# Performance work log

Measured on AMD Instinct MI355X. Metric: run time of the kernel, lower is better.

Reference implementation:

```python
import jax, jax.numpy as jnp
import numpy as np

L, WIDTH, H, B, S = 3, 4, 512, 32, 512
NHW = 2
CIN = (WIDTH + 1) * H


def _windows(padded, off0):
    # padded: [B, S+2W, H] -> [B, S, (W+1)*H], window k covers padded[:, off0+k : off0+k+S]
    return jnp.concatenate([padded[:, off0 + k: off0 + k + S] for k in range(WIDTH + 1)], axis=-1)


def _highway(x, Ws, bs):
    # Ws: [NHW, H, 2H], bs: [NHW, 2H]. AllenNLP Highway: gate*x + (1-gate)*relu(nonlin)
    for j in range(NHW):
        proj = x @ Ws[j] + bs[j]
        nonlin, gate = jnp.split(proj, 2, axis=-1)
        g = jax.nn.sigmoid(gate)
        x = g * x + (1.0 - g) * jax.nn.relu(nonlin)
    return x


def setup_inputs() -> dict:
    key = jax.random.key(0)
    ks = jax.random.split(key, 13)
    inputs = jax.random.normal(ks[0], (B, S, H), dtype=jnp.float32)
    mask = jnp.ones((B, S), dtype=jnp.int32)
    fwd_pads = jax.random.normal(ks[1], (L, WIDTH, H), dtype=jnp.float32)
    bwd_pads = jax.random.normal(ks[2], (L, WIDTH, H), dtype=jnp.float32)
    fwd_W = jax.random.normal(ks[3], (L, CIN, H), dtype=jnp.float32) * 0.02
    bwd_W = jax.random.normal(ks[4], (L, CIN, H), dtype=jnp.float32) * 0.02
    fwd_b = jnp.zeros((L, H), dtype=jnp.float32)
    bwd_b = jnp.zeros((L, H), dtype=jnp.float32)
    fwd_hw_W = jax.random.normal(ks[5], (L, NHW, H, 2 * H), dtype=jnp.float32) * 0.04
    bwd_hw_W = jax.random.normal(ks[6], (L, NHW, H, 2 * H), dtype=jnp.float32) * 0.04
    fwd_hw_b = jnp.zeros((L, NHW, 2 * H), dtype=jnp.float32)
    bwd_hw_b = jnp.zeros((L, NHW, 2 * H), dtype=jnp.float32)
    return {"inputs": inputs, "mask": mask, "fwd_pads": fwd_pads, "bwd_pads": bwd_pads,
            "fwd_W": fwd_W, "fwd_b": fwd_b, "bwd_W": bwd_W, "bwd_b": bwd_b,
            "fwd_hw_W": fwd_hw_W, "fwd_hw_b": fwd_hw_b, "bwd_hw_W": bwd_hw_W, "bwd_hw_b": bwd_hw_b}


def reference(inputs, mask, fwd_pads, bwd_pads, fwd_W, fwd_b, bwd_W, bwd_b,
              fwd_hw_W, fwd_hw_b, bwd_hw_W, bwd_hw_b):
    f_seq = inputs
    b_seq = inputs
    outs = []
    for i in range(L):
        pf = jnp.broadcast_to(fwd_pads[i], (B, WIDTH, H))
        pb = jnp.broadcast_to(bwd_pads[i], (B, WIDTH, H))
        pad_f = jnp.concatenate([pf, f_seq, pb], axis=1)  # [B, S+2W, H]
        pad_b = jnp.concatenate([pf, b_seq, pb], axis=1)
        # forward windows start at offset 0 (positions t-W..t); backward at offset W (t..t+W)
        f_in = _windows(pad_f, 0)       # [B, S, (W+1)*H]
        b_in = _windows(pad_b, WIDTH)
        f = jax.nn.relu(f_in @ fwd_W[i] + fwd_b[i])
        f = _highway(f, fwd_hw_W[i], fwd_hw_b[i])
        b = jax.nn.relu(b_in @ bwd_W[i] + bwd_b[i])
        b = _highway(b, bwd_hw_W[i], bwd_hw_b[i])
        f_seq, b_seq = f, b
        outs.append(jnp.concatenate([f, b], axis=-1))
    return jnp.stack(outs, axis=0)  # [L, B, S, 2H]
```

## Files before the change

kernel.cpp:

```cpp
#include <hip/hip_runtime.h>
#include <hip/hip_fp16.h>
#include <cstdint>
#include <cstddef>

constexpr int HD   = 512;
constexpr int SQ   = 512;
constexpr int NB   = 32;
constexpr int LAY  = 3;
constexpr int WID  = 4;
constexpr int KIN  = (WID + 1) * HD;
constexpr int PROW = SQ + 2 * WID;
constexpr int MR   = NB * SQ;

typedef _Float16 f16x8 __attribute__((ext_vector_type(8)));
typedef float    f32x4 __attribute__((ext_vector_type(4)));

__device__ __forceinline__ void gld16(void* lds, const void* g) {
  __builtin_amdgcn_global_load_lds(
      (__attribute__((address_space(1))) void*)(g),
      (__attribute__((address_space(3))) void*)(lds),
      16, 0, 0);
}

__global__ void transpose_w(const float* __restrict__ in, _Float16* __restrict__ out,
                            int R, int C) {
  __shared__ float tile[32][33];
  const size_t base = (size_t)blockIdx.z * R * C;
  const int r0 = blockIdx.y * 32, c0 = blockIdx.x * 32;
  const int tx = threadIdx.x, ty = threadIdx.y;
#pragma unroll
  for (int j = 0; j < 32; j += 8)
    tile[ty + j][tx] = in[base + (size_t)(r0 + ty + j) * C + (c0 + tx)];
  __syncthreads();
#pragma unroll
  for (int j = 0; j < 32; j += 8)
    out[base + (size_t)(c0 + ty + j) * R + (r0 + tx)] = (_Float16)tile[tx][ty + j];
}

__global__ void init_interior(const float4* __restrict__ in,
                              _Float16* __restrict__ padF, _Float16* __restrict__ padB) {
  const size_t idx = (size_t)blockIdx.x * 256 + threadIdx.x;
  float4 v = in[idx];
  const size_t e = idx * 4;
  const int h = (int)(e & (HD - 1));
  const size_t bt = e >> 9;
  const int t = (int)(bt & (SQ - 1));
  const int b = (int)(bt >> 9);
  const size_t o = ((size_t)(b * PROW + WID + t)) * HD + h;
  union { _Float16 hh[4]; uint2 u; } pk;
  pk.hh[0] = (_Float16)v.x; pk.hh[1] = (_Float16)v.y;
  pk.hh[2] = (_Float16)v.z; pk.hh[3] = (_Float16)v.w;
  *(uint2*)&padF[o] = pk.u;
  *(uint2*)&padB[o] = pk.u;
}

__global__ void fill_pads(const float* __restrict__ fpad, const float* __restrict__ bpad,
                          _Float16* __restrict__ padF, _Float16* __restrict__ padB) {
  const int idx = blockIdx.x * 256 + threadIdx.x;
  const int h  = idx & (HD - 1);
  const int w  = (idx >> 9) & 3;
  const int b  = (idx >> 11) & 31;
  const int fb = idx >> 16;
  const float v = fb ? bpad[w * HD + h] : fpad[w * HD + h];
  const int row = fb ? (SQ + WID + w) : w;
  const size_t o = ((size_t)(b * PROW + row)) * HD + h;
  const _Float16 hv = (_Float16)v;
  padF[o] = hv;
  padB[o] = hv;
}

__global__ __launch_bounds__(256)
void conv_gemm(const _Float16* __restrict__ padFp, const _Float16* __restrict__ padBp,
               const _Float16* __restrict__ WtF, const _Float16* __restrict__ WtB,
               const float* __restrict__ biasF, const float* __restrict__ biasB,
               _Float16* __restrict__ tF, _Float16* __restrict__ tB) {
  const int id   = blockIdx.x;
  const int xcd  = id & 7;
  const int dir  = xcd >> 2;
  const int xl   = xcd & 3;
  const int slot = id >> 3;
  const int nt   = slot & 3;
  const int mg   = slot >> 2;
  const int mt   = xl + 4 * mg;

  const _Float16* pad = dir ? padBp : padFp;
  const _Float16* Wt  = dir ? WtB : WtF;
  const float* bias   = dir ? biasB : biasF;
  _Float16* outT      = dir ? tB : tF;
  const int off = dir ? WID : 0;

  const int m0 = mt * 128;
  const int n0 = nt * 128;
  const int b  = m0 >> 9;
  const int t0 = m0 & (SQ - 1);

  __shared__ alignas(16) _Float16 Asm[128 * 64];
  __shared__ alignas(16) _Float16 Bsm[128 * 64];

  const int tid  = threadIdx.x;
  const int lane = tid & 63, wv = tid >> 6;
  const int wr = (wv >> 1) * 64, wc = (wv & 1) * 64;
  const int lr = lane & 15, q = lane >> 4;
  const int srow = tid >> 3;
  const int clog = (tid & 7) ^ (srow & 7);
  const int goff = clog * 8;

  f32x4 acc[4][4] = {};

  const size_t arow0 = (size_t)(b * PROW + t0 + off);

#pragma unroll 2
  for (int k0 = 0; k0 < KIN; k0 += 64) {
    const int kseg = k0 >> 9;
    const int h0 = k0 & (HD - 1);
    const _Float16* Ab = pad + (arow0 + kseg) * (size_t)HD + h0;
    const _Float16* Bb = Wt + (size_t)n0 * KIN + k0;
    __syncthreads();
#pragma unroll
    for (int j = 0; j < 4; ++j) {
      gld16(&Asm[j * 2048 + tid * 8], Ab + (size_t)(j * 32 + srow) * HD + goff);
      gld16(&Bsm[j * 2048 + tid * 8], Bb + (size_t)(j * 32 + srow) * KIN + goff);
    }
    __syncthreads();

#pragma unroll
    for (int h = 0; h < 2; ++h) {
      f16x8 af[4], bf[4];
#pragma unroll
      for (int r = 0; r < 4; ++r) {
        const int row = wr + r * 16 + lr;
        const int ch = ((h << 2) | q) ^ (lr & 7);
        af[r] = *(const f16x8*)&Asm[row * 64 + ch * 8];
      }
#pragma unroll
      for (int c = 0; c < 4; ++c) {
        const int row = wc + c * 16 + lr;
        const int ch = ((h << 2) | q) ^ (lr & 7);
        bf[c] = *(const f16x8*)&Bsm[row * 64 + ch * 8];
      }
#pragma unroll
      for (int r = 0; r < 4; ++r)
#pragma unroll
        for (int c = 0; c < 4; ++c)
          acc[r][c] = __builtin_amdgcn_mfma_f32_16x16x32_f16(af[r], bf[c], acc[r][c], 0, 0, 0);
    }
  }

#pragma unroll
  for (int c = 0; c < 4; ++c) {
    const int ng = n0 + wc + c * 16 + lr;
    const float bv = bias[ng];
#pragma unroll
    for (int r = 0; r < 4; ++r) {
      const int mg2 = m0 + wr + r * 16 + q * 4;
#pragma unroll
      for (int g = 0; g < 4; ++g) {
        float v = acc[r][c][g] + bv;
        v = v > 0.f ? v : 0.f;
        outT[(size_t)(mg2 + g) * HD + ng] = (_Float16)v;
      }
    }
  }
}

__global__ __launch_bounds__(256)
void hw_gemm(const _Float16* __restrict__ xF, const _Float16* __restrict__ xB,
             const _Float16* __restrict__ WtFp, const _Float16* __restrict__ WtBp,
             const float* __restrict__ bFp, const float* __restrict__ bBp,
             _Float16* __restrict__ oFp, _Float16* __restrict__ oBp,
             float* __restrict__ out32, int mode) {
  const int id   = blockIdx.x;
  const int xcd  = id & 7;
  const int dir  = xcd >> 2;
  const int xl   = xcd & 3;
  const int slot = id >> 3;
  const int nt   = slot & 7;
  const int mg   = slot >> 3;
  const int mt   = xl + 4 * mg;

  const _Float16* x  = dir ? xB : xF;
  const _Float16* Wt = dir ? WtBp : WtFp;
  const float* bias  = dir ? bBp : bFp;
  _Float16* oh       = dir ? oBp : oFp;

  const int m0 = mt * 128;
  const int n0 = nt * 64;

  __shared__ alignas(16) _Float16 Asm[128 * 64];
  __shared__ alignas(16) _Float16 Bn[64 * 64];
  __shared__ alignas(16) _Float16 Bg[64 * 64];

  const int tid  = threadIdx.x;
  const int lane = tid & 63, wv = tid >> 6;
  const int wr = (wv >> 1) * 64, wc = (wv & 1) * 32;
  const int lr = lane & 15, q = lane >> 4;
  const int srow = tid >> 3;
  const int clog = (tid & 7) ^ (srow & 7);
  const int goff = clog * 8;

  f32x4 an[4][2] = {};
  f32x4 ag[4][2] = {};
  _Float16 xv[4][2][4] = {};

  for (int k0 = 0; k0 < HD; k0 += 64) {
    const _Float16* Ab  = x + (size_t)m0 * HD + k0;
    const _Float16* Bnb = Wt + (size_t)n0 * HD + k0;
    const _Float16* Bgb = Wt + (size_t)(HD + n0) * HD + k0;
    __syncthreads();
#pragma unroll
    for (int j = 0; j < 4; ++j)
      gld16(&Asm[j * 2048 + tid * 8], Ab + (size_t)(j * 32 + srow) * HD + goff);
#pragma unroll
    for (int j = 0; j < 2; ++j) {
      gld16(&Bn[j * 2048 + tid * 8], Bnb + (size_t)(j * 32 + srow) * HD + goff);
      gld16(&Bg[j * 2048 + tid * 8], Bgb + (size_t)(j * 32 + srow) * HD + goff);
    }
    __syncthreads();

    if (k0 == n0) {
#pragma unroll
      for (int r = 0; r < 4; ++r)
#pragma unroll
        for (int c = 0; c < 2; ++c)
#pragma unroll
          for (int g = 0; g < 4; ++g) {
            const int row = wr + r * 16 + q * 4 + g;
            const int col = wc + c * 16 + lr;
            xv[r][c][g] = Asm[row * 64 + ((((col >> 3) ^ (row & 7)) << 3) | (col & 7))];
          }
    }

#pragma unroll
    for (int h = 0; h < 2; ++h) {
      f16x8 af[4], bn[2], bg[2];
#pragma unroll
      for (int r = 0; r < 4; ++r) {
        const int row = wr + r * 16 + lr;
        const int ch = ((h << 2) | q) ^ (lr & 7);
        af[r] = *(const f16x8*)&Asm[row * 64 + ch * 8];
      }
#pragma unroll
      for (int c = 0; c < 2; ++c) {
        const int row = wc + c * 16 + lr;
        const int ch = ((h << 2) | q) ^ (lr & 7);
        bn[c] = *(const f16x8*)&Bn[row * 64 + ch * 8];
        bg[c] = *(const f16x8*)&Bg[row * 64 + ch * 8];
      }
#pragma unroll
      for (int r = 0; r < 4; ++r)
#pragma unroll
        for (int c = 0; c < 2; ++c) {
          an[r][c] = __builtin_amdgcn_mfma_f32_16x16x32_f16(af[r], bn[c], an[r][c], 0, 0, 0);
          ag[r][c] = __builtin_amdgcn_mfma_f32_16x16x32_f16(af[r], bg[c], ag[r][c], 0, 0, 0);
        }
    }
  }

#pragma unroll
  for (int c = 0; c < 2; ++c) {
    const int ng = n0 + wc + c * 16 + lr;
    const float bnv = bias[ng];
    const float bgv = bias[HD + ng];
#pragma unroll
    for (int r = 0; r < 4; ++r) {
      const int mg2 = m0 + wr + r * 16 + q * 4;
#pragma unroll
      for (int g = 0; g < 4; ++g) {
        const int row = mg2 + g;
        float nl = an[r][c][g] + bnv;
        nl = nl > 0.f ? nl : 0.f;
        const float gz = ag[r][c][g] + bgv;
        const float gate = 1.f / (1.f + __expf(-gz));
        const float xvf = (float)xv[r][c][g];
        const float o = gate * xvf + (1.f - gate) * nl;
        if (mode == 0) {
          oh[(size_t)row * HD + ng] = (_Float16)o;
        } else {
          const int bb = row >> 9, tt = row & (SQ - 1);
          oh[((size_t)(bb * PROW + WID + tt)) * HD + ng] = (_Float16)o;
          out32[(size_t)row * (2 * HD) + dir * HD + ng] = o;
        }
      }
    }
  }
}

extern "C" void kernel_launch(void* const* d_in, const int* in_sizes, int n_in,
                              void* d_out, int out_size, void* d_ws, size_t ws_size,
                              hipStream_t stream) {
  const float* inputs   = (const float*)d_in[0];
  const float* fwd_pads = (const float*)d_in[2];
  const float* bwd_pads = (const float*)d_in[3];
  const float* fwd_W    = (const float*)d_in[4];
  const float* fwd_b    = (const float*)d_in[5];
  const float* bwd_W    = (const float*)d_in[6];
  const float* bwd_b    = (const float*)d_in[7];
  const float* fwd_hw_W = (const float*)d_in[8];
  const float* fwd_hw_b = (const float*)d_in[9];
  const float* bwd_hw_W = (const float*)d_in[10];
  const float* bwd_hw_b = (const float*)d_in[11];
  float* out = (float*)d_out;

  char* p = (char*)d_ws;
  auto take = [&](size_t n) { char* r = p; p += (n + 255) & ~(size_t)255; return r; };

  _Float16* padF = (_Float16*)take((size_t)NB * PROW * HD * 2);
  _Float16* padB = (_Float16*)take((size_t)NB * PROW * HD * 2);
  _Float16* tF   = (_Float16*)take((size_t)MR * HD * 2);
  _Float16* tB   = (_Float16*)take((size_t)MR * HD * 2);
  _Float16* uF   = (_Float16*)take((size_t)MR * HD * 2);
  _Float16* uB   = (_Float16*)take((size_t)MR * HD * 2);
  _Float16* WtcF = (_Float16*)take((size_t)LAY * HD * KIN * 2);
  _Float16* WtcB = (_Float16*)take((size_t)LAY * HD * KIN * 2);
  _Float16* WthF = (_Float16*)take((size_t)LAY * 2 * (2 * HD) * HD * 2);
  _Float16* WthB = (_Float16*)take((size_t)LAY * 2 * (2 * HD) * HD * 2);

  transpose_w<<<dim3(HD / 32, KIN / 32, LAY), dim3(32, 8), 0, stream>>>(fwd_W, WtcF, KIN, HD);
  transpose_w<<<dim3(HD / 32, KIN / 32, LAY), dim3(32, 8), 0, stream>>>(bwd_W, WtcB, KIN, HD);
  transpose_w<<<dim3((2 * HD) / 32, HD / 32, LAY * 2), dim3(32, 8), 0, stream>>>(fwd_hw_W, WthF, HD, 2 * HD);
  transpose_w<<<dim3((2 * HD) / 32, HD / 32, LAY * 2), dim3(32, 8), 0, stream>>>(bwd_hw_W, WthB, HD, 2 * HD);

  init_interior<<<(NB * SQ * HD / 4) / 256, 256, 0, stream>>>((const float4*)inputs, padF, padB);

  for (int i = 0; i < LAY; ++i) {
    fill_pads<<<512, 256, 0, stream>>>(fwd_pads + (size_t)i * WID * HD,
                                       bwd_pads + (size_t)i * WID * HD, padF, padB);
    conv_gemm<<<dim3(1024), 256, 0, stream>>>(
        padF, padB,
        WtcF + (size_t)i * HD * KIN, WtcB + (size_t)i * HD * KIN,
        fwd_b + (size_t)i * HD, bwd_b + (size_t)i * HD, tF, tB);
    hw_gemm<<<dim3(2048), 256, 0, stream>>>(
        tF, tB,
        WthF + (size_t)(i * 2 + 0) * (2 * HD) * HD, WthB + (size_t)(i * 2 + 0) * (2 * HD) * HD,
        fwd_hw_b + (size_t)(i * 2 + 0) * (2 * HD), bwd_hw_b + (size_t)(i * 2 + 0) * (2 * HD),
        uF, uB, nullptr, 0);
    hw_gemm<<<dim3(2048), 256, 0, stream>>>(
        uF, uB,
        WthF + (size_t)(i * 2 + 1) * (2 * HD) * HD, WthB + (size_t)(i * 2 + 1) * (2 * HD) * HD,
        fwd_hw_b + (size_t)(i * 2 + 1) * (2 * HD), bwd_hw_b + (size_t)(i * 2 + 1) * (2 * HD),
        padF, padB, out + (size_t)i * MR * (2 * HD), 1);
  }
}
```

Measured before the change: 1.071 ms.

## Enlarge highway GEMM tiles, stage epilogues through LDS, and batch setup kernels

The highway GEMM now uses 256x64 output tiles, each wave covering 64 rows by all 64 columns, and launches half as many blocks. Both GEMM epilogues write results to swizzled LDS first, then issue 16-byte coalesced global stores. The highway residual is now read from global memory in the epilogue instead of being captured from LDS in the K loop. Setup is batched: the forward and backward weight transposes share one launch, and the pad rows for all layers are filled once into per-layer pad buffers, which removes the per-layer fill kernel. The last layer skips writing the unused padded copy. The trade-offs are more LDS per block and the gate pre-activation being rounded to fp16 before the sigmoid.

```diff
diff --git a/kernel.cpp b/kernel.cpp
--- a/kernel.cpp
+++ b/kernel.cpp
@@ -11,6 +11,7 @@
 constexpr int KIN  = (WID + 1) * HD;
 constexpr int PROW = SQ + 2 * WID;
 constexpr int MR   = NB * SQ;
+constexpr int PSTR = NB * PROW * HD;
 
 typedef _Float16 f16x8 __attribute__((ext_vector_type(8)));
 typedef float    f32x4 __attribute__((ext_vector_type(4)));
@@ -22,10 +23,15 @@
       16, 0, 0);
 }
 
-__global__ void transpose_w(const float* __restrict__ in, _Float16* __restrict__ out,
-                            int R, int C) {
+__global__ void transpose_w2(const float* __restrict__ inF, const float* __restrict__ inB,
+                             _Float16* __restrict__ outF, _Float16* __restrict__ outB,
+                             int R, int C, int nsl) {
   __shared__ float tile[32][33];
-  const size_t base = (size_t)blockIdx.z * R * C;
+  const int z = blockIdx.z;
+  const float* in = (z < nsl) ? inF : inB;
+  _Float16* out   = (z < nsl) ? outF : outB;
+  const int sl    = (z < nsl) ? z : z - nsl;
+  const size_t base = (size_t)sl * R * C;
   const int r0 = blockIdx.y * 32, c0 = blockIdx.x * 32;
   const int tx = threadIdx.x, ty = threadIdx.y;
 #pragma unroll
@@ -54,16 +60,17 @@
   *(uint2*)&padB[o] = pk.u;
 }
 
-__global__ void fill_pads(const float* __restrict__ fpad, const float* __restrict__ bpad,
-                          _Float16* __restrict__ padF, _Float16* __restrict__ padB) {
+__global__ void fill_all_pads(const float* __restrict__ fpads, const float* __restrict__ bpads,
+                              _Float16* __restrict__ padF, _Float16* __restrict__ padB) {
   const int idx = blockIdx.x * 256 + threadIdx.x;
   const int h  = idx & (HD - 1);
   const int w  = (idx >> 9) & 3;
   const int b  = (idx >> 11) & 31;
-  const int fb = idx >> 16;
-  const float v = fb ? bpad[w * HD + h] : fpad[w * HD + h];
+  const int fb = (idx >> 16) & 1;
+  const int l  = idx >> 17;
+  const float v = fb ? bpads[l * WID * HD + w * HD + h] : fpads[l * WID * HD + w * HD + h];
   const int row = fb ? (SQ + WID + w) : w;
-  const size_t o = ((size_t)(b * PROW + row)) * HD + h;
+  const size_t o = (size_t)l * PSTR + ((size_t)(b * PROW + row)) * HD + h;
   const _Float16 hv = (_Float16)v;
   padF[o] = hv;
   padB[o] = hv;
@@ -94,8 +101,9 @@
   const int b  = m0 >> 9;
   const int t0 = m0 & (SQ - 1);
 
-  __shared__ alignas(16) _Float16 Asm[128 * 64];
-  __shared__ alignas(16) _Float16 Bsm[128 * 64];
+  __shared__ alignas(16) _Float16 SM[128 * 128];
+  _Float16* Asm = SM;
+  _Float16* Bsm = SM + 8192;
 
   const int tid  = threadIdx.x;
   const int lane = tid & 63, wv = tid >> 6;
@@ -126,18 +134,13 @@
 #pragma unroll
     for (int h = 0; h < 2; ++h) {
       f16x8 af[4], bf[4];
-#pragma unroll
-      for (int r = 0; r < 4; ++r) {
-        const int row = wr + r * 16 + lr;
-        const int ch = ((h << 2) | q) ^ (lr & 7);
-        af[r] = *(const f16x8*)&Asm[row * 64 + ch * 8];
-      }
-#pragma unroll
-      for (int c = 0; c < 4; ++c) {
-        const int row = wc + c * 16 + lr;
-        const int ch = ((h << 2) | q) ^ (lr & 7);
-        bf[c] = *(const f16x8*)&Bsm[row * 64 + ch * 8];
-      }
+      const int ch = ((h << 2) | q) ^ (lr & 7);
+#pragma unroll
+      for (int r = 0; r < 4; ++r)
+        af[r] = *(const f16x8*)&Asm[(wr + r * 16 + lr) * 64 + ch * 8];
+#pragma unroll
+      for (int c = 0; c < 4; ++c)
+        bf[c] = *(const f16x8*)&Bsm[(wc + c * 16 + lr) * 64 + ch * 8];
 #pragma unroll
       for (int r = 0; r < 4; ++r)
 #pragma unroll
@@ -146,20 +149,31 @@
     }
   }
 
+  __syncthreads();
 #pragma unroll
   for (int c = 0; c < 4; ++c) {
-    const int ng = n0 + wc + c * 16 + lr;
-    const float bv = bias[ng];
-#pragma unroll
-    for (int r = 0; r < 4; ++r) {
-      const int mg2 = m0 + wr + r * 16 + q * 4;
+    const int col = wc + c * 16 + lr;
+    const float bv = bias[n0 + col];
+#pragma unroll
+    for (int r = 0; r < 4; ++r)
 #pragma unroll
       for (int g = 0; g < 4; ++g) {
+        const int row = wr + r * 16 + q * 4 + g;
+        const int pc = (col >> 3) ^ (row & 7);
         float v = acc[r][c][g] + bv;
         v = v > 0.f ? v : 0.f;
-        outT[(size_t)(mg2 + g) * HD + ng] = (_Float16)v;
+        SM[row * 128 + pc * 8 + (col & 7)] = (_Float16)v;
       }
-    }
+  }
+  __syncthreads();
+#pragma unroll
+  for (int j = 0; j < 8; ++j) {
+    const int cid = j * 256 + tid;
+    const int row = cid >> 4;
+    const int gc = cid & 15;
+    const int pc = gc ^ (row & 7);
+    f16x8 v8 = *(const f16x8*)&SM[row * 128 + pc * 8];
+    *(f16x8*)&outT[(size_t)(m0 + row) * HD + n0 + gc * 8] = v8;
   }
 }
 
@@ -183,32 +197,32 @@
   const float* bias  = dir ? bBp : bFp;
   _Float16* oh       = dir ? oBp : oFp;
 
-  const int m0 = mt * 128;
+  const int m0 = mt * 256;
   const int n0 = nt * 64;
 
-  __shared__ alignas(16) _Float16 Asm[128 * 64];
-  __shared__ alignas(16) _Float16 Bn[64 * 64];
-  __shared__ alignas(16) _Float16 Bg[64 * 64];
+  __shared__ alignas(16) _Float16 SM[32768];
+  _Float16* Asm = SM;
+  _Float16* Bn  = SM + 16384;
+  _Float16* Bg  = SM + 20480;
 
   const int tid  = threadIdx.x;
   const int lane = tid & 63, wv = tid >> 6;
-  const int wr = (wv >> 1) * 64, wc = (wv & 1) * 32;
   const int lr = lane & 15, q = lane >> 4;
   const int srow = tid >> 3;
   const int clog = (tid & 7) ^ (srow & 7);
   const int goff = clog * 8;
 
-  f32x4 an[4][2] = {};
-  f32x4 ag[4][2] = {};
-  _Float16 xv[4][2][4] = {};
-
+  f32x4 an[4][4] = {};
+  f32x4 ag[4][4] = {};
+
+#pragma unroll 2
   for (int k0 = 0; k0 < HD; k0 += 64) {
     const _Float16* Ab  = x + (size_t)m0 * HD + k0;
     const _Float16* Bnb = Wt + (size_t)n0 * HD + k0;
     const _Float16* Bgb = Wt + (size_t)(HD + n0) * HD + k0;
     __syncthreads();
 #pragma unroll
-    for (int j = 0; j < 4; ++j)
+    for (int j = 0; j < 8; ++j)
       gld16(&Asm[j * 2048 + tid * 8], Ab + (size_t)(j * 32 + srow) * HD + goff);
 #pragma unroll
     for (int j = 0; j < 2; ++j) {
@@ -217,70 +231,77 @@
     }
     __syncthreads();
 
-    if (k0 == n0) {
+#pragma unroll
+    for (int h = 0; h < 2; ++h) {
+      const int ch = ((h << 2) | q) ^ (lr & 7);
+      f16x8 af[4], bn[4], bg[4];
 #pragma unroll
       for (int r = 0; r < 4; ++r)
-#pragma unroll
-        for (int c = 0; c < 2; ++c)
-#pragma unroll
-          for (int g = 0; g < 4; ++g) {
-            const int row = wr + r * 16 + q * 4 + g;
-            const int col = wc + c * 16 + lr;
-            xv[r][c][g] = Asm[row * 64 + ((((col >> 3) ^ (row & 7)) << 3) | (col & 7))];
-          }
-    }
-
-#pragma unroll
-    for (int h = 0; h < 2; ++h) {
-      f16x8 af[4], bn[2], bg[2];
-#pragma unroll
-      for (int r = 0; r < 4; ++r) {
-        const int row = wr + r * 16 + lr;
-        const int ch = ((h << 2) | q) ^ (lr & 7);
-        af[r] = *(const f16x8*)&Asm[row * 64 + ch * 8];
+        af[r] = *(const f16x8*)&Asm[(wv * 64 + r * 16 + lr) * 64 + ch * 8];
+#pragma unroll
+      for (int c = 0; c < 4; ++c) {
+        bn[c] = *(const f16x8*)&Bn[(c * 16 + lr) * 64 + ch * 8];
+        bg[c] = *(const f16x8*)&Bg[(c * 16 + lr) * 64 + ch * 8];
       }
 #pragma unroll
-      for (int c = 0; c < 2; ++c) {
-        const int row = wc + c * 16 + lr;
-        const int ch = ((h << 2) | q) ^ (lr & 7);
-        bn[c] = *(const f16x8*)&Bn[row * 64 + ch * 8];
-        bg[c] = *(const f16x8*)&Bg[row * 64 + ch * 8];
-      }
-#pragma unroll
       for (int r = 0; r < 4; ++r)
 #pragma unroll
-        for (int c = 0; c < 2; ++c) {
+        for (int c = 0; c < 4; ++c) {
           an[r][c] = __builtin_amdgcn_mfma_f32_16x16x32_f16(af[r], bn[c], an[r][c], 0, 0, 0);
           ag[r][c] = __builtin_amdgcn_mfma_f32_16x16x32_f16(af[r], bg[c], ag[r][c], 0, 0, 0);
         }
     }
   }
 
-#pragma unroll
-  for (int c = 0; c < 2; ++c) {
-    const int ng = n0 + wc + c * 16 + lr;
-    const float bnv = bias[ng];
-    const float bgv = bias[HD + ng];
-#pragma unroll
-    for (int r = 0; r < 4; ++r) {
-      const int mg2 = m0 + wr + r * 16 + q * 4;
+  __syncthreads();
+#pragma unroll
+  for (int c = 0; c < 4; ++c) {
+    const int col = c * 16 + lr;
+    const float bnv = bias[n0 + col];
+    const float bgv = bias[HD + n0 + col];
+#pragma unroll
+    for (int r = 0; r < 4; ++r)
 #pragma unroll
       for (int g = 0; g < 4; ++g) {
-        const int row = mg2 + g;
+        const int row = wv * 64 + r * 16 + q * 4 + g;
+        const int pc = (col >> 3) ^ (row & 7);
+        const int a = row * 64 + pc * 8 + (col & 7);
         float nl = an[r][c][g] + bnv;
         nl = nl > 0.f ? nl : 0.f;
-        const float gz = ag[r][c][g] + bgv;
-        const float gate = 1.f / (1.f + __expf(-gz));
-        const float xvf = (float)xv[r][c][g];
-        const float o = gate * xvf + (1.f - gate) * nl;
-        if (mode == 0) {
-          oh[(size_t)row * HD + ng] = (_Float16)o;
-        } else {
-          const int bb = row >> 9, tt = row & (SQ - 1);
-          oh[((size_t)(bb * PROW + WID + tt)) * HD + ng] = (_Float16)o;
-          out32[(size_t)row * (2 * HD) + dir * HD + ng] = o;
-        }
+        SM[a] = (_Float16)nl;
+        SM[16384 + a] = (_Float16)(ag[r][c][g] + bgv);
       }
+  }
+  __syncthreads();
+#pragma unroll
+  for (int j = 0; j < 8; ++j) {
+    const int cid = j * 256 + tid;
+    const int row = cid >> 3;
+    const int gc = cid & 7;
+    const int pc = gc ^ (row & 7);
+    f16x8 nl8 = *(const f16x8*)&SM[row * 64 + pc * 8];
+    f16x8 gz8 = *(const f16x8*)&SM[16384 + row * 64 + pc * 8];
+    const int xrow = m0 + row;
+    f16x8 xv8 = *(const f16x8*)&x[(size_t)xrow * HD + n0 + gc * 8];
+    f16x8 o8;
+    float of[8];
+#pragma unroll
+    for (int e = 0; e < 8; ++e) {
+      const float gt = 1.f / (1.f + __expf(-(float)gz8[e]));
+      const float o = gt * (float)xv8[e] + (1.f - gt) * (float)nl8[e];
+      of[e] = o;
+      o8[e] = (_Float16)o;
+    }
+    if (mode == 0) {
+      *(f16x8*)&oh[(size_t)xrow * HD + n0 + gc * 8] = o8;
+    } else {
+      if (mode == 1) {
+        const int bb = xrow >> 9, tt = xrow & (SQ - 1);
+        *(f16x8*)&oh[((size_t)(bb * PROW + WID + tt)) * HD + n0 + gc * 8] = o8;
+      }
+      float* op = out32 + (size_t)xrow * (2 * HD) + dir * HD + n0 + gc * 8;
+      *(float4*)op = make_float4(of[0], of[1], of[2], of[3]);
+      *(float4*)(op + 4) = make_float4(of[4], of[5], of[6], of[7]);
     }
   }
 }
@@ -304,8 +325,8 @@
   char* p = (char*)d_ws;
   auto take = [&](size_t n) { char* r = p; p += (n + 255) & ~(size_t)255; return r; };
 
-  _Float16* padF = (_Float16*)take((size_t)NB * PROW * HD * 2);
-  _Float16* padB = (_Float16*)take((size_t)NB * PROW * HD * 2);
+  _Float16* padF = (_Float16*)take((size_t)LAY * PSTR * 2);
+  _Float16* padB = (_Float16*)take((size_t)LAY * PSTR * 2);
   _Float16* tF   = (_Float16*)take((size_t)MR * HD * 2);
   _Float16* tB   = (_Float16*)take((size_t)MR * HD * 2);
   _Float16* uF   = (_Float16*)take((size_t)MR * HD * 2);
@@ -315,29 +336,34 @@
   _Float16* WthF = (_Float16*)take((size_t)LAY * 2 * (2 * HD) * HD * 2);
   _Float16* WthB = (_Float16*)take((size_t)LAY * 2 * (2 * HD) * HD * 2);
 
-  transpose_w<<<dim3(HD / 32, KIN / 32, LAY), dim3(32, 8), 0, stream>>>(fwd_W, WtcF, KIN, HD);
-  transpose_w<<<dim3(HD / 32, KIN / 32, LAY), dim3(32, 8), 0, stream>>>(bwd_W, WtcB, KIN, HD);
-  transpose_w<<<dim3((2 * HD) / 32, HD / 32, LAY * 2), dim3(32, 8), 0, stream>>>(fwd_hw_W, WthF, HD, 2 * HD);
-  transpose_w<<<dim3((2 * HD) / 32, HD / 32, LAY * 2), dim3(32, 8), 0, stream>>>(bwd_hw_W, WthB, HD, 2 * HD);
+  transpose_w2<<<dim3(HD / 32, KIN / 32, 2 * LAY), dim3(32, 8), 0, stream>>>(
+      fwd_W, bwd_W, WtcF, WtcB, KIN, HD, LAY);
+  transpose_w2<<<dim3((2 * HD) / 32, HD / 32, 2 * LAY * 2), dim3(32, 8), 0, stream>>>(
+      fwd_hw_W, bwd_hw_W, WthF, WthB, HD, 2 * HD, LAY * 2);
 
   init_interior<<<(NB * SQ * HD / 4) / 256, 256, 0, stream>>>((const float4*)inputs, padF, padB);
+  fill_all_pads<<<(LAY * 2 * NB * WID * HD) / 256, 256, 0, stream>>>(fwd_pads, bwd_pads, padF, padB);
 
   for (int i = 0; i < LAY; ++i) {
-    fill_pads<<<512, 256, 0, stream>>>(fwd_pads + (size_t)i * WID * HD,
-                                       bwd_pads + (size_t)i * WID * HD, padF, padB);
+    _Float16* pF = padF + (size_t)i * PSTR;
+    _Float16* pB = padB + (size_t)i * PSTR;
+    const int nx = (i + 1 < LAY) ? (i + 1) : 0;
+    _Float16* nF = padF + (size_t)nx * PSTR;
+    _Float16* nB = padB + (size_t)nx * PSTR;
+
     conv_gemm<<<dim3(1024), 256, 0, stream>>>(
-        padF, padB,
+        pF, pB,
         WtcF + (size_t)i * HD * KIN, WtcB + (size_t)i * HD * KIN,
         fwd_b + (size_t)i * HD, bwd_b + (size_t)i * HD, tF, tB);
-    hw_gemm<<<dim3(2048), 256, 0, stream>>>(
+    hw_gemm<<<dim3(1024), 256, 0, stream>>>(
         tF, tB,
         WthF + (size_t)(i * 2 + 0) * (2 * HD) * HD, WthB + (size_t)(i * 2 + 0) * (2 * HD) * HD,
         fwd_hw_b + (size_t)(i * 2 + 0) * (2 * HD), bwd_hw_b + (size_t)(i * 2 + 0) * (2 * HD),
         uF, uB, nullptr, 0);
-    hw_gemm<<<dim3(2048), 256, 0, stream>>>(
+    hw_gemm<<<dim3(1024), 256, 0, stream>>>(
         uF, uB,
         WthF + (size_t)(i * 2 + 1) * (2 * HD) * HD, WthB + (size_t)(i * 2 + 1) * (2 * HD) * HD,
         fwd_hw_b + (size_t)(i * 2 + 1) * (2 * HD), bwd_hw_b + (size_t)(i * 2 + 1) * (2 * HD),
-        padF, padB, out + (size_t)i * MR * (2 * HD), 1);
-  }
-}
+        nF, nB, out + (size_t)i * MR * (2 * HD), (i + 1 < LAY) ? 1 : 2);
+  }
+}
```

Result: faster. 981.1 us (-8.4%).
